# Performance work log

Measured on AMD Instinct MI355X. Metric: run time of the kernel, lower is better.

Reference implementation:

```python
import jax, jax.numpy as jnp
import numpy as np

B, S, D, H = 4, 2048, 1024, 16
DH = D // H  # 64
EPS = 1e-5


def setup_inputs() -> dict:
    key = jax.random.key(0)
    ks = jax.random.split(key, 6)
    scale = 0.02
    return {
        "x": jax.random.normal(ks[0], (B, S, D), dtype=jnp.float32),
        "Wq": jax.random.normal(ks[1], (H, D, DH), dtype=jnp.float32) * scale,
        "Wk": jax.random.normal(ks[2], (H, D, DH), dtype=jnp.float32) * scale,
        "Wv": jax.random.normal(ks[3], (H, D, DH), dtype=jnp.float32) * scale,
        "Wo": jax.random.normal(ks[4], (D, D), dtype=jnp.float32) * scale,
        "bo": jnp.zeros((D,), dtype=jnp.float32),
        "gamma": jnp.ones((D,), dtype=jnp.float32),
        "beta": jnp.zeros((D,), dtype=jnp.float32),
    }


def reference(x, Wq, Wk, Wv, Wo, bo, gamma, beta):
    # Per-head projections, stacked across heads: [B,H,S,DH]
    q = jnp.einsum("bsd,hdk->bhsk", x, Wq)
    k = jnp.einsum("bsd,hdk->bhsk", x, Wk)
    v = jnp.einsum("bsd,hdk->bhsk", x, Wv)
    inv_scale = 1.0 / jnp.sqrt(jnp.float32(DH))  # key.size(-1) == head_dim
    scores = jnp.einsum("bhqk,bhsk->bhqs", q, k) * inv_scale  # [B,H,S,S]
    attn = jax.nn.softmax(scores, axis=-1)
    ctx = jnp.einsum("bhqs,bhsk->bhqk", attn, v)  # [B,H,S,DH]
    # concat heads -> [B,S,D]
    concat = jnp.transpose(ctx, (0, 2, 1, 3)).reshape(B, S, D)
    proj = concat @ Wo + bo  # fc_out (Wo stored as [in,out])
    added = proj + x  # residual add
    mu = jnp.mean(added, axis=-1, keepdims=True)
    var = jnp.mean(jnp.square(added - mu), axis=-1, keepdims=True)
    normed = (added - mu) * jax.lax.rsqrt(var + EPS)
    return normed * gamma + beta
```

## Files before the change

### kernel.cpp

```cpp
#include <hip/hip_runtime.h>
#include <hip/hip_bf16.h>
#include <stdint.h>

#define DEV __device__ __forceinline__

typedef short s16x8 __attribute__((ext_vector_type(8)));
typedef float f32x4 __attribute__((ext_vector_type(4)));
typedef int i32x4 __attribute__((ext_vector_type(4)));

DEV void async_load16(const void* g, void* l) {
  __builtin_amdgcn_global_load_lds((void __attribute__((address_space(1)))*)(g),
                                   (void __attribute__((address_space(3)))*)(l),
                                   16, 0, 0);
}

DEV unsigned pack_bf16x2(float a, float b) {
  __hip_bfloat162 h = __float22bfloat162_rn(make_float2(a, b));
  union { __hip_bfloat162 h2; unsigned u; } cv;
  cv.h2 = h;
  return cv.u;
}

__global__ __launch_bounds__(256) void cast_x_kernel(const float* __restrict__ in,
                                                     __hip_bfloat16* __restrict__ out, int n4) {
  int i = blockIdx.x * 256 + threadIdx.x;
  if (i >= n4) return;
  float4 v = ((const float4*)in)[i];
  alignas(8) __hip_bfloat16 t[4] = {__float2bfloat16(v.x), __float2bfloat16(v.y),
                                    __float2bfloat16(v.z), __float2bfloat16(v.w)};
  *(uint2*)(out + (size_t)i * 4) = *(const uint2*)t;
}

__global__ __launch_bounds__(256) void transpose_cast_kernel(const float* __restrict__ src,
                                                             __hip_bfloat16* __restrict__ dst,
                                                             int R, int C, float scale) {
  __shared__ float tile[64][65];
  const int r0 = blockIdx.x * 64, c0 = blockIdx.y * 64, bt = blockIdx.z;
  const int tc = threadIdx.x & 63, tr = threadIdx.x >> 6;
  const float* sp = src + (size_t)bt * R * C;
#pragma unroll
  for (int rr = 0; rr < 64; rr += 4)
    tile[tr + rr][tc] = sp[(size_t)(r0 + tr + rr) * C + c0 + tc];
  __syncthreads();
  __hip_bfloat16* dp = dst + (size_t)bt * R * C;
#pragma unroll
  for (int rr = 0; rr < 64; rr += 4) {
    int cc = tr + rr;
    dp[(size_t)(c0 + cc) * R + r0 + tc] = __float2bfloat16(tile[tc][cc] * scale);
  }
}

__global__ __launch_bounds__(256) void qkv_transpose_kernel(const float* __restrict__ Wq,
                                                            const float* __restrict__ Wk,
                                                            const float* __restrict__ Wv,
                                                            __hip_bfloat16* __restrict__ dst,
                                                            float qscale) {
  __shared__ float tile[64][65];
  const int z = blockIdx.z, which = z >> 4, bt = z & 15;
  const int r0 = blockIdx.x * 64;
  const int tc = threadIdx.x & 63, tr = threadIdx.x >> 6;
  const float* src = (which == 0) ? Wq : (which == 1) ? Wk : Wv;
  const float scale = (which == 0) ? qscale : 1.0f;
  const float* sp = src + (size_t)bt * 1024 * 64;
#pragma unroll
  for (int rr = 0; rr < 64; rr += 4)
    tile[tr + rr][tc] = sp[(size_t)(r0 + tr + rr) * 64 + tc];
  __syncthreads();
  __hip_bfloat16* dp = dst + (size_t)z * 1024 * 64;
#pragma unroll
  for (int rr = 0; rr < 64; rr += 4) {
    int cc = tr + rr;
    dp[(size_t)(cc)*1024 + r0 + tc] = __float2bfloat16(tile[tc][cc] * scale);
  }
}

template <int MODE>
__global__ __launch_bounds__(256) void gemm128(const __hip_bfloat16* __restrict__ A,
                                               const __hip_bfloat16* __restrict__ Bt,
                                               void* __restrict__ out0,
                                               void* __restrict__ out1,
                                               void* __restrict__ out2,
                                               const float* __restrict__ bias,
                                               const float* __restrict__ resid,
                                               int M, int N, int K) {
  __shared__ __hip_bfloat16 As[128 * 32];
  __shared__ __hip_bfloat16 Bs[128 * 32];
  const int tid = threadIdx.x;
  const int lane = tid & 63, w = tid >> 6;
  const int lr = lane & 15, lq = lane >> 4;
  const int wm = w >> 1, wn = w & 1;
  const int nlin = blockIdx.x + gridDim.x * blockIdx.y;
  const int xcd = nlin & 7, slot = nlin >> 3;
  const int bx = slot >> 3;
  const int by = xcd * 8 + (slot & 7);
  const int m0 = by * 128, n0 = bx * 128;

  const f32x4 fz = {0.f, 0.f, 0.f, 0.f};
  f32x4 acc[4][4];
#pragma unroll
  for (int i = 0; i < 4; i++)
#pragma unroll
    for (int j = 0; j < 4; j++) acc[i][j] = fz;

  const int kiters = K >> 5;
  for (int kt = 0; kt < kiters; kt++) {
    __syncthreads();
#pragma unroll
    for (int r = 0; r < 2; r++) {
      const int c = r * 256 + tid;
      const int row = c >> 2, kc = c & 3;
      async_load16((const short*)A + (size_t)(m0 + row) * K + kt * 32 + kc * 8,
                   (char*)As + (r * 256 + (tid & 0xC0)) * 16);
      async_load16((const short*)Bt + (size_t)(n0 + row) * K + kt * 32 + kc * 8,
                   (char*)Bs + (r * 256 + (tid & 0xC0)) * 16);
    }
    __syncthreads();
    const short* Ap = (const short*)As;
    const short* Bp = (const short*)Bs;
    s16x8 av[4], bv[4];
#pragma unroll
    for (int i = 0; i < 4; i++)
      av[i] = *(const s16x8*)(Ap + (wm * 64 + i * 16 + lr) * 32 + lq * 8);
#pragma unroll
    for (int j = 0; j < 4; j++)
      bv[j] = *(const s16x8*)(Bp + (wn * 64 + j * 16 + lr) * 32 + lq * 8);
#pragma unroll
    for (int i = 0; i < 4; i++)
#pragma unroll
      for (int j = 0; j < 4; j++)
        acc[i][j] = __builtin_amdgcn_mfma_f32_16x16x32_bf16(av[i], bv[j], acc[i][j], 0, 0, 0);
  }

  if constexpr (MODE == 0) {
    if (n0 < 2048) {
      __hip_bfloat16* dst01 = (__hip_bfloat16*)((n0 < 1024) ? out0 : out1);
#pragma unroll
      for (int i = 0; i < 4; i++)
#pragma unroll
        for (int j = 0; j < 4; j++)
#pragma unroll
          for (int r = 0; r < 4; r++) {
            const int row = m0 + wm * 64 + i * 16 + lq * 4 + r;
            const int col = n0 + wn * 64 + j * 16 + lr;
            const int bb = row >> 11, s = row & 2047;
            const int colq = col & 1023;
            dst01[((((size_t)bb * 16 + (colq >> 6)) * 2048 + s) << 6) + (col & 63)] =
                __float2bfloat16(acc[i][j][r]);
          }
    } else {
#pragma unroll
      for (int i = 0; i < 4; i++)
#pragma unroll
        for (int j = 0; j < 4; j++) {
          const int row0 = m0 + wm * 64 + i * 16 + lq * 4;
          const int col = (n0 - 2048) + wn * 64 + j * 16 + lr;
          const int bb = row0 >> 11, s0 = row0 & 2047;
          alignas(8) __hip_bfloat16 t4[4] = {
              __float2bfloat16(acc[i][j][0]), __float2bfloat16(acc[i][j][1]),
              __float2bfloat16(acc[i][j][2]), __float2bfloat16(acc[i][j][3])};
          *(uint2*)((__hip_bfloat16*)out2 + (size_t)bb * 2097152 + (size_t)col * 2048 + s0) =
              *(const uint2*)t4;
        }
    }
  } else {
#pragma unroll
    for (int i = 0; i < 4; i++)
#pragma unroll
      for (int j = 0; j < 4; j++)
#pragma unroll
        for (int r = 0; r < 4; r++) {
          const int row = m0 + wm * 64 + i * 16 + lq * 4 + r;
          const int col = n0 + wn * 64 + j * 16 + lr;
          const size_t idx = (size_t)row * 1024 + col;
          ((float*)out0)[idx] = acc[i][j][r] + bias[col] + resid[idx];
        }
  }
}

__global__ __launch_bounds__(256, 4) void flash_kernel(const __hip_bfloat16* __restrict__ Qg,
                                                       const __hip_bfloat16* __restrict__ Kg,
                                                       const __hip_bfloat16* __restrict__ Vtg,
                                                       __hip_bfloat16* __restrict__ Og) {
  __shared__ alignas(16) char smem[32768];
  float* xch = (float*)smem;
  const int tid = threadIdx.x;
  const int lane = tid & 63, w = tid >> 6;
  const int lr = lane & 15, lq = lane >> 4;
  const int qp = w >> 1;
  const int kvh = w & 1;
  const int hb = blockIdx.x, qt = blockIdx.y;
  const int h = hb >> 2, b = hb & 3;
  const size_t bh = (size_t)b * 16 + h;
  const short* Qbase = (const short*)Qg + (bh * 2048 + (size_t)qt * 64) * 64;
  const short* Kbh = (const short*)Kg + bh * 2048 * 64;
  const short* Vbh = (const short*)Vtg + bh * 64 * 2048;

  const int rbase = (lr >> 2) * 8 + (lr & 3);
  const int gk = lr & 7;

  s16x8 qb[2][2];
#pragma unroll
  for (int ntl = 0; ntl < 2; ntl++)
#pragma unroll
    for (int ks = 0; ks < 2; ks++)
      qb[ntl][ks] =
          *(const s16x8*)(Qbase + ((qp * 2 + ntl) * 16 + lr) * 64 + ks * 32 + lq * 8);

  s16x8 vones;
#pragma unroll
  for (int e = 0; e < 8; e++) vones[e] = (short)0x3F80;

  const f32x4 fz = {0.f, 0.f, 0.f, 0.f};
  f32x4 o[2][4];
  f32x4 ol[2];
#pragma unroll
  for (int i = 0; i < 2; i++) {
    ol[i] = fz;
#pragma unroll
    for (int j = 0; j < 4; j++) o[i][j] = fz;
  }

  auto stage = [&](int sel, int kb) {
    char* Kl = smem + sel * 16384;
    char* Vl = Kl + 8192;
    const short* Ksrc = Kbh + kb * 64 * 64;
#pragma unroll
    for (int r = 0; r < 2; r++) {
      int c = r * 256 + tid;
      int row = c >> 3, ck = c & 7;
      int g = (row & 3) | (((row >> 3) & 1) << 2);
      async_load16(Ksrc + row * 64 + (ck ^ g) * 8, Kl + (r * 256 + (tid & 0xC0)) * 16);
    }
#pragma unroll
    for (int r = 0; r < 2; r++) {
      int c = r * 256 + tid;
      int row = c >> 3, ck = c & 7;
      async_load16(Vbh + (size_t)row * 2048 + kb * 64 + ((ck ^ (row & 7))) * 8,
                   Vl + (r * 256 + (tid & 0xC0)) * 16);
    }
  };

  stage(0, 0);
  __syncthreads();

  for (int kb = 0; kb < 32; kb++) {
    const int cur = kb & 1;
    if (kb + 1 < 32) stage(cur ^ 1, kb + 1);

    const short* Kp = (const short*)(smem + cur * 16384);
    const short* Vp = (const short*)(smem + cur * 16384 + 8192);

    union { i32x4 i; s16x8 s; } pa[2];
#pragma unroll
    for (int mt = 0; mt < 2; mt++) {
      const int kvrow = kvh * 32 + mt * 4 + rbase;
      s16x8 kf0 = *(const s16x8*)(Kp + kvrow * 64 + (((0 * 4 + lq) ^ gk)) * 8);
      s16x8 kf1 = *(const s16x8*)(Kp + kvrow * 64 + (((1 * 4 + lq) ^ gk)) * 8);
#pragma unroll
      for (int ntl = 0; ntl < 2; ntl++) {
        f32x4 st = fz;
        st = __builtin_amdgcn_mfma_f32_16x16x32_bf16(kf0, qb[ntl][0], st, 0, 0, 0);
        st = __builtin_amdgcn_mfma_f32_16x16x32_bf16(kf1, qb[ntl][1], st, 0, 0, 0);
        float e0 = __builtin_amdgcn_exp2f(st[0]);
        float e1 = __builtin_amdgcn_exp2f(st[1]);
        float e2 = __builtin_amdgcn_exp2f(st[2]);
        float e3 = __builtin_amdgcn_exp2f(st[3]);
        pa[ntl].i[mt * 2 + 0] = (int)pack_bf16x2(e0, e1);
        pa[ntl].i[mt * 2 + 1] = (int)pack_bf16x2(e2, e3);
      }
    }
    __builtin_amdgcn_s_setprio(1);
#pragma unroll
    for (int ntl = 0; ntl < 2; ntl++)
      ol[ntl] = __builtin_amdgcn_mfma_f32_16x16x32_bf16(pa[ntl].s, vones, ol[ntl], 0, 0, 0);
#pragma unroll
    for (int ndh = 0; ndh < 4; ndh++) {
      int vrow = ndh * 16 + lr;
      s16x8 vb = *(const s16x8*)(Vp + vrow * 64 + (((kvh * 4 + lq) ^ (vrow & 7))) * 8);
#pragma unroll
      for (int ntl = 0; ntl < 2; ntl++)
        o[ntl][ndh] =
            __builtin_amdgcn_mfma_f32_16x16x32_bf16(pa[ntl].s, vb, o[ntl][ndh], 0, 0, 0);
    }
    __builtin_amdgcn_s_setprio(0);

    __syncthreads();
  }

  float* slot = xch + w * 1280;
  if (kvh == 0) {
#pragma unroll
    for (int ndh = 0; ndh < 4; ndh++)
      *(f32x4*)(slot + ndh * 256 + lane * 4) = o[1][ndh];
    *(f32x4*)(slot + 1024 + lane * 4) = ol[1];
  } else {
#pragma unroll
    for (int ndh = 0; ndh < 4; ndh++)
      *(f32x4*)(slot + ndh * 256 + lane * 4) = o[0][ndh];
    *(f32x4*)(slot + 1024 + lane * 4) = ol[0];
  }
  __syncthreads();
  const float* ps = xch + (w ^ 1) * 1280;
  if (kvh == 0) {
#pragma unroll
    for (int ndh = 0; ndh < 4; ndh++)
      o[0][ndh] += *(const f32x4*)(ps + ndh * 256 + lane * 4);
    f32x4 lt = ol[0] + *(const f32x4*)(ps + 1024 + lane * 4);
#pragma unroll
    for (int r = 0; r < 4; r++) {
      float inv = __builtin_amdgcn_rcpf(lt[r]);
      int rowg = qt * 64 + w * 16 + lq * 4 + r;
#pragma unroll
      for (int ndh = 0; ndh < 4; ndh++)
        Og[((size_t)b * 2048 + rowg) * 1024 + h * 64 + ndh * 16 + lr] =
            __float2bfloat16(o[0][ndh][r] * inv);
    }
  } else {
#pragma unroll
    for (int ndh = 0; ndh < 4; ndh++)
      o[1][ndh] += *(const f32x4*)(ps + ndh * 256 + lane * 4);
    f32x4 lt = ol[1] + *(const f32x4*)(ps + 1024 + lane * 4);
#pragma unroll
    for (int r = 0; r < 4; r++) {
      float inv = __builtin_amdgcn_rcpf(lt[r]);
      int rowg = qt * 64 + w * 16 + lq * 4 + r;
#pragma unroll
      for (int ndh = 0; ndh < 4; ndh++)
        Og[((size_t)b * 2048 + rowg) * 1024 + h * 64 + ndh * 16 + lr] =
            __float2bfloat16(o[1][ndh][r] * inv);
    }
  }
}

__global__ __launch_bounds__(256) void ln_kernel(const float* __restrict__ tmp,
                                                 const float* __restrict__ gamma,
                                                 const float* __restrict__ beta,
                                                 float* __restrict__ out) {
  const int row = blockIdx.x, tid = threadIdx.x;
  const int lane = tid & 63, w = tid >> 6;
  const float* rp = tmp + (size_t)row * 1024;
  float4 v = ((const float4*)rp)[tid];
  float s = v.x + v.y + v.z + v.w;
  float ss = v.x * v.x + v.y * v.y + v.z * v.z + v.w * v.w;
#pragma unroll
  for (int off = 32; off >= 1; off >>= 1) {
    s += __shfl_xor(s, off);
    ss += __shfl_xor(ss, off);
  }
  __shared__ float red[8];
  if (lane == 0) {
    red[w] = s;
    red[4 + w] = ss;
  }
  __syncthreads();
  s = red[0] + red[1] + red[2] + red[3];
  ss = red[4] + red[5] + red[6] + red[7];
  const float mu = s * (1.0f / 1024.0f);
  const float var = ss * (1.0f / 1024.0f) - mu * mu;
  const float rstd = rsqrtf(var + 1e-5f);
  float4 g = ((const float4*)gamma)[tid];
  float4 be = ((const float4*)beta)[tid];
  float4 ov;
  ov.x = (v.x - mu) * rstd * g.x + be.x;
  ov.y = (v.y - mu) * rstd * g.y + be.y;
  ov.z = (v.z - mu) * rstd * g.z + be.z;
  ov.w = (v.w - mu) * rstd * g.w + be.w;
  ((float4*)(out + (size_t)row * 1024))[tid] = ov;
}

extern "C" void kernel_launch(void* const* d_in, const int* in_sizes, int n_in,
                              void* d_out, int out_size, void* d_ws, size_t ws_size,
                              hipStream_t stream) {
  (void)in_sizes; (void)n_in; (void)out_size; (void)ws_size;
  const float* x = (const float*)d_in[0];
  const float* Wq = (const float*)d_in[1];
  const float* Wk = (const float*)d_in[2];
  const float* Wv = (const float*)d_in[3];
  const float* Wo = (const float*)d_in[4];
  const float* bo = (const float*)d_in[5];
  const float* gamma = (const float*)d_in[6];
  const float* beta = (const float*)d_in[7];
  float* out = (float*)d_out;
  char* ws = (char*)d_ws;

  __hip_bfloat16* xb = (__hip_bfloat16*)(ws + 0);
  __hip_bfloat16* wqkvT = (__hip_bfloat16*)(ws + 16777216);
  __hip_bfloat16* woT = (__hip_bfloat16*)(ws + 23068672);
  __hip_bfloat16* Q = (__hip_bfloat16*)(ws + 25165824);
  __hip_bfloat16* Kt = (__hip_bfloat16*)(ws + 41943040);
  __hip_bfloat16* Vt = (__hip_bfloat16*)(ws + 58720256);
  __hip_bfloat16* cc = (__hip_bfloat16*)(ws + 75497472);
  float* tmp = (float*)(ws + 25165824);

  cast_x_kernel<<<8192, 256, 0, stream>>>(x, xb, 2097152);
  qkv_transpose_kernel<<<dim3(16, 1, 48), 256, 0, stream>>>(Wq, Wk, Wv, wqkvT,
                                                            0.125f * 1.44269504088896f);
  transpose_cast_kernel<<<dim3(16, 16, 1), 256, 0, stream>>>(Wo, woT, 1024, 1024, 1.0f);

  gemm128<0><<<dim3(24, 64), 256, 0, stream>>>(xb, wqkvT, Q, Kt, Vt, nullptr, nullptr,
                                               8192, 3072, 1024);

  flash_kernel<<<dim3(64, 32), 256, 0, stream>>>(Q, Kt, Vt, cc);

  gemm128<2><<<dim3(8, 64), 256, 0, stream>>>(cc, woT, tmp, nullptr, nullptr, bo, x,
                                              8192, 1024, 1024);
  ln_kernel<<<8192, 256, 0, stream>>>(tmp, gamma, beta, out);
}
```

Before: 303.2 us.

## Double-buffer GEMM LDS tiles with staggered per-wave compute phases

Converts the 128x128 bf16 GEMM main loop from single-buffered load-then-compute into a double-buffered pipeline. Each k-iteration is split into four barrier-separated phases. Each phase issues one sub-tile of the next iteration's loads, and only the wave whose operands have landed (tracked with vmcnt(2)) runs its MFMAs, at raised priority. The aim is to overlap global-to-LDS async loads with MFMA work and avoid full-tile waits. The cost is twice the LDS per block, four barriers per iteration, and MFMA work serialized across waves within a block.

```diff
diff --git a/kernel.cpp b/kernel.cpp
--- a/kernel.cpp
+++ b/kernel.cpp
@@ -83,8 +83,8 @@
                                                const float* __restrict__ bias,
                                                const float* __restrict__ resid,
                                                int M, int N, int K) {
-  __shared__ __hip_bfloat16 As[128 * 32];
-  __shared__ __hip_bfloat16 Bs[128 * 32];
+  __shared__ __hip_bfloat16 As[2][128 * 32];
+  __shared__ __hip_bfloat16 Bs[2][128 * 32];
   const int tid = threadIdx.x;
   const int lane = tid & 63, w = tid >> 6;
   const int lr = lane & 15, lq = lane >> 4;
@@ -102,21 +102,21 @@
 #pragma unroll
     for (int j = 0; j < 4; j++) acc[i][j] = fz;
 
-  const int kiters = K >> 5;
-  for (int kt = 0; kt < kiters; kt++) {
-    __syncthreads();
-#pragma unroll
-    for (int r = 0; r < 2; r++) {
-      const int c = r * 256 + tid;
-      const int row = c >> 2, kc = c & 3;
-      async_load16((const short*)A + (size_t)(m0 + row) * K + kt * 32 + kc * 8,
-                   (char*)As + (r * 256 + (tid & 0xC0)) * 16);
-      async_load16((const short*)Bt + (size_t)(n0 + row) * K + kt * 32 + kc * 8,
-                   (char*)Bs + (r * 256 + (tid & 0xC0)) * 16);
-    }
-    __syncthreads();
-    const short* Ap = (const short*)As;
-    const short* Bp = (const short*)Bs;
+  auto stageA = [&](int sel, int kt, int r) {
+    const int c = r * 256 + tid;
+    const int row = c >> 2, kc = c & 3;
+    async_load16((const short*)A + (size_t)(m0 + row) * K + kt * 32 + kc * 8,
+                 (char*)As[sel] + (r * 256 + (tid & 0xC0)) * 16);
+  };
+  auto stageB = [&](int sel, int kt, int r) {
+    const int c = r * 256 + tid;
+    const int row = c >> 2, kc = c & 3;
+    async_load16((const short*)Bt + (size_t)(n0 + row) * K + kt * 32 + kc * 8,
+                 (char*)Bs[sel] + (r * 256 + (tid & 0xC0)) * 16);
+  };
+  auto compute = [&](int cur) {
+    const short* Ap = (const short*)As[cur];
+    const short* Bp = (const short*)Bs[cur];
     s16x8 av[4], bv[4];
 #pragma unroll
     for (int i = 0; i < 4; i++)
@@ -124,11 +124,44 @@
 #pragma unroll
     for (int j = 0; j < 4; j++)
       bv[j] = *(const s16x8*)(Bp + (wn * 64 + j * 16 + lr) * 32 + lq * 8);
+    __builtin_amdgcn_s_setprio(1);
 #pragma unroll
     for (int i = 0; i < 4; i++)
 #pragma unroll
       for (int j = 0; j < 4; j++)
         acc[i][j] = __builtin_amdgcn_mfma_f32_16x16x32_bf16(av[i], bv[j], acc[i][j], 0, 0, 0);
+    __builtin_amdgcn_s_setprio(0);
+  };
+
+  const int kiters = K >> 5;
+  stageA(0, 0, 0);
+  stageB(0, 0, 0);
+  stageB(0, 0, 1);
+  stageA(0, 0, 1);
+
+  for (int kt = 0; kt < kiters; kt++) {
+    const int cur = kt & 1, nxt = cur ^ 1;
+    const int ktn = (kt + 1 < kiters) ? kt + 1 : kt;
+    asm volatile("s_waitcnt vmcnt(2)" ::: "memory");
+    __builtin_amdgcn_s_barrier();
+    __builtin_amdgcn_sched_barrier(0);
+    stageA(nxt, ktn, 0);
+    if (w == 0) compute(cur);
+    asm volatile("s_waitcnt vmcnt(2)" ::: "memory");
+    __builtin_amdgcn_s_barrier();
+    __builtin_amdgcn_sched_barrier(0);
+    stageB(nxt, ktn, 0);
+    if (w == 1) compute(cur);
+    asm volatile("s_waitcnt vmcnt(2)" ::: "memory");
+    __builtin_amdgcn_s_barrier();
+    __builtin_amdgcn_sched_barrier(0);
+    stageB(nxt, ktn, 1);
+    if (w == 2) compute(cur);
+    asm volatile("s_waitcnt vmcnt(2)" ::: "memory");
+    __builtin_amdgcn_s_barrier();
+    __builtin_amdgcn_sched_barrier(0);
+    stageA(nxt, ktn, 1);
+    if (w == 3) compute(cur);
   }
 
   if constexpr (MODE == 0) {
```

Result: slower. 359.0 us (+18.4%).

## Double GEMM K-tile and single-buffer flash kernel for higher occupancy

Applied to the files above, without the earlier changes.

The GEMM kernel now stages a 64-wide K slice per iteration instead of 32, halving the number of barrier-separated load/compute rounds and issuing twice as many MFMAs between syncs. The flash attention kernel drops its double-buffered K/V staging in favour of a single buffer, shrinks LDS, and raises the launch-bounds occupancy hint from 4 to 7 blocks. This trades explicit prefetch overlap in attention for more resident waves to hide latency, and it risks losing load/compute overlap plus register pressure under the tighter bound.

```diff
diff --git a/kernel.cpp b/kernel.cpp
--- a/kernel.cpp
+++ b/kernel.cpp
@@ -83,8 +83,8 @@
                                                const float* __restrict__ bias,
                                                const float* __restrict__ resid,
                                                int M, int N, int K) {
-  __shared__ __hip_bfloat16 As[128 * 32];
-  __shared__ __hip_bfloat16 Bs[128 * 32];
+  __shared__ __hip_bfloat16 As[128 * 64];
+  __shared__ __hip_bfloat16 Bs[128 * 64];
   const int tid = threadIdx.x;
   const int lane = tid & 63, w = tid >> 6;
   const int lr = lane & 15, lq = lane >> 4;
@@ -102,33 +102,40 @@
 #pragma unroll
     for (int j = 0; j < 4; j++) acc[i][j] = fz;
 
-  const int kiters = K >> 5;
+  const int kiters = K >> 6;
   for (int kt = 0; kt < kiters; kt++) {
     __syncthreads();
 #pragma unroll
-    for (int r = 0; r < 2; r++) {
+    for (int r = 0; r < 4; r++) {
       const int c = r * 256 + tid;
-      const int row = c >> 2, kc = c & 3;
-      async_load16((const short*)A + (size_t)(m0 + row) * K + kt * 32 + kc * 8,
+      const int row = c >> 3, ck = c & 7;
+      async_load16((const short*)A + (size_t)(m0 + row) * K + kt * 64 + ck * 8,
                    (char*)As + (r * 256 + (tid & 0xC0)) * 16);
-      async_load16((const short*)Bt + (size_t)(n0 + row) * K + kt * 32 + kc * 8,
+      async_load16((const short*)Bt + (size_t)(n0 + row) * K + kt * 64 + ck * 8,
                    (char*)Bs + (r * 256 + (tid & 0xC0)) * 16);
     }
     __syncthreads();
     const short* Ap = (const short*)As;
     const short* Bp = (const short*)Bs;
-    s16x8 av[4], bv[4];
+    s16x8 av[4][2], bv[4][2];
 #pragma unroll
     for (int i = 0; i < 4; i++)
-      av[i] = *(const s16x8*)(Ap + (wm * 64 + i * 16 + lr) * 32 + lq * 8);
+#pragma unroll
+      for (int ks = 0; ks < 2; ks++)
+        av[i][ks] = *(const s16x8*)(Ap + (wm * 64 + i * 16 + lr) * 64 + ks * 32 + lq * 8);
 #pragma unroll
     for (int j = 0; j < 4; j++)
-      bv[j] = *(const s16x8*)(Bp + (wn * 64 + j * 16 + lr) * 32 + lq * 8);
-#pragma unroll
-    for (int i = 0; i < 4; i++)
-#pragma unroll
-      for (int j = 0; j < 4; j++)
-        acc[i][j] = __builtin_amdgcn_mfma_f32_16x16x32_bf16(av[i], bv[j], acc[i][j], 0, 0, 0);
+#pragma unroll
+      for (int ks = 0; ks < 2; ks++)
+        bv[j][ks] = *(const s16x8*)(Bp + (wn * 64 + j * 16 + lr) * 64 + ks * 32 + lq * 8);
+#pragma unroll
+    for (int ks = 0; ks < 2; ks++)
+#pragma unroll
+      for (int i = 0; i < 4; i++)
+#pragma unroll
+        for (int j = 0; j < 4; j++)
+          acc[i][j] =
+              __builtin_amdgcn_mfma_f32_16x16x32_bf16(av[i][ks], bv[j][ks], acc[i][j], 0, 0, 0);
   }
 
   if constexpr (MODE == 0) {
@@ -177,11 +184,11 @@
   }
 }
 
-__global__ __launch_bounds__(256, 4) void flash_kernel(const __hip_bfloat16* __restrict__ Qg,
+__global__ __launch_bounds__(256, 7) void flash_kernel(const __hip_bfloat16* __restrict__ Qg,
                                                        const __hip_bfloat16* __restrict__ Kg,
                                                        const __hip_bfloat16* __restrict__ Vtg,
                                                        __hip_bfloat16* __restrict__ Og) {
-  __shared__ alignas(16) char smem[32768];
+  __shared__ alignas(16) char smem[20480];
   float* xch = (float*)smem;
   const int tid = threadIdx.x;
   const int lane = tid & 63, w = tid >> 6;
@@ -220,9 +227,9 @@
     for (int j = 0; j < 4; j++) o[i][j] = fz;
   }
 
-  auto stage = [&](int sel, int kb) {
-    char* Kl = smem + sel * 16384;
-    char* Vl = Kl + 8192;
+  auto stage = [&](int kb) {
+    char* Kl = smem;
+    char* Vl = smem + 8192;
     const short* Ksrc = Kbh + kb * 64 * 64;
 #pragma unroll
     for (int r = 0; r < 2; r++) {
@@ -240,15 +247,12 @@
     }
   };
 
-  stage(0, 0);
-  __syncthreads();
-
   for (int kb = 0; kb < 32; kb++) {
-    const int cur = kb & 1;
-    if (kb + 1 < 32) stage(cur ^ 1, kb + 1);
-
-    const short* Kp = (const short*)(smem + cur * 16384);
-    const short* Vp = (const short*)(smem + cur * 16384 + 8192);
+    stage(kb);
+    __syncthreads();
+
+    const short* Kp = (const short*)smem;
+    const short* Vp = (const short*)(smem + 8192);
 
     union { i32x4 i; s16x8 s; } pa[2];
 #pragma unroll
```

Result: slower. 669.2 us (+120.7%).

## Replace QKV projection GEMM with 256x128 triple-buffered async-LDS pipelined kernel

Applied to the files above, without the earlier changes.

Adds a dedicated QKV GEMM with 256x128 tiles, 512 threads, a 64-wide K step and three LDS stages. Global-to-LDS loads are XOR-swizzled to avoid bank conflicts and are split so A and B loads interleave with MFMA halves. Blocks are remapped so each XCD works on its own band of rows, and MFMA sections run at raised wave priority. The aim is to hide memory latency and improve reuse in the largest GEMM, at the cost of more LDS per block (144 KB) and lower occupancy.

```diff
diff --git a/kernel.cpp b/kernel.cpp
--- a/kernel.cpp
+++ b/kernel.cpp
@@ -71,6 +71,140 @@
   for (int rr = 0; rr < 64; rr += 4) {
     int cc = tr + rr;
     dp[(size_t)(cc)*1024 + r0 + tc] = __float2bfloat16(tile[tc][cc] * scale);
+  }
+}
+
+__global__ __launch_bounds__(512, 2) void gemm256_qkv(const __hip_bfloat16* __restrict__ A,
+                                                      const __hip_bfloat16* __restrict__ Bt,
+                                                      __hip_bfloat16* __restrict__ outQ,
+                                                      __hip_bfloat16* __restrict__ outK,
+                                                      __hip_bfloat16* __restrict__ outV,
+                                                      int M, int N, int K) {
+  __shared__ __hip_bfloat16 lds[3 * 24576];
+  const int tid = threadIdx.x;
+  const int lane = tid & 63, w = tid >> 6;
+  const int lr = lane & 15, lq = lane >> 4;
+  const int wm = w >> 1, wn = w & 1;
+  const int gk = lr & 7;
+  const int nlin = blockIdx.x + gridDim.x * blockIdx.y;
+  const int xcd = nlin & 7, sid = nlin >> 3;
+  const int bx = sid >> 2;
+  const int by = xcd * 4 + (sid & 3);
+  const int m0 = by * 256, n0 = bx * 128;
+
+  const f32x4 fz = {0.f, 0.f, 0.f, 0.f};
+  f32x4 acc[4][4];
+#pragma unroll
+  for (int i = 0; i < 4; i++)
+#pragma unroll
+    for (int j = 0; j < 4; j++) acc[i][j] = fz;
+
+  auto stageA = [&](int tt, int sl) {
+#pragma unroll
+    for (int r = 0; r < 4; r++) {
+      const int c = r * 512 + tid;
+      const int row = c >> 3, ck = c & 7;
+      async_load16((const short*)A + (size_t)(m0 + row) * K + tt * 64 + ((ck ^ (row & 7)) * 8),
+                   (char*)lds + sl * 49152 + (r * 512 + (tid & 0x1C0)) * 16);
+    }
+  };
+  auto stageB = [&](int tt, int sl) {
+#pragma unroll
+    for (int r = 0; r < 2; r++) {
+      const int c = r * 512 + tid;
+      const int row = c >> 3, ck = c & 7;
+      async_load16((const short*)Bt + (size_t)(n0 + row) * K + tt * 64 + ((ck ^ (row & 7)) * 8),
+                   (char*)lds + sl * 49152 + 32768 + (r * 512 + (tid & 0x1C0)) * 16);
+    }
+  };
+
+  stageA(0, 0); stageB(0, 0);
+  stageA(1, 1); stageB(1, 1);
+
+  const int kiters = K >> 6;
+  int slot = 0;
+  for (int t = 0; t < kiters; t++) {
+    const short* Ap = (const short*)lds + slot * 24576;
+    const short* Bp = Ap + 16384;
+    const int tt = (t + 2 < kiters) ? t + 2 : kiters - 1;
+    int sln = slot + 2; if (sln >= 3) sln -= 3;
+
+    asm volatile("s_waitcnt vmcnt(6)\n\ts_barrier" ::: "memory");
+
+    stageA(tt, sln);
+    s16x8 bv[4][2], av0[2][2];
+#pragma unroll
+    for (int j = 0; j < 4; j++)
+#pragma unroll
+      for (int ks = 0; ks < 2; ks++)
+        bv[j][ks] = *(const s16x8*)(Bp + (wn * 64 + j * 16 + lr) * 64 + (((ks * 4 + lq) ^ gk)) * 8);
+#pragma unroll
+    for (int i = 0; i < 2; i++)
+#pragma unroll
+      for (int ks = 0; ks < 2; ks++)
+        av0[i][ks] = *(const s16x8*)(Ap + (wm * 64 + i * 16 + lr) * 64 + (((ks * 4 + lq) ^ gk)) * 8);
+    __builtin_amdgcn_s_setprio(1);
+#pragma unroll
+    for (int ks = 0; ks < 2; ks++)
+#pragma unroll
+      for (int i = 0; i < 2; i++)
+#pragma unroll
+      for (int j = 0; j < 4; j++)
+        acc[i][j] = __builtin_amdgcn_mfma_f32_16x16x32_bf16(av0[i][ks], bv[j][ks], acc[i][j], 0, 0, 0);
+    __builtin_amdgcn_s_setprio(0);
+    asm volatile("s_barrier" ::: "memory");
+
+    stageB(tt, sln);
+    s16x8 av1[2][2];
+#pragma unroll
+    for (int i = 0; i < 2; i++)
+#pragma unroll
+      for (int ks = 0; ks < 2; ks++)
+        av1[i][ks] =
+            *(const s16x8*)(Ap + (wm * 64 + (2 + i) * 16 + lr) * 64 + (((ks * 4 + lq) ^ gk)) * 8);
+    __builtin_amdgcn_s_setprio(1);
+#pragma unroll
+    for (int ks = 0; ks < 2; ks++)
+#pragma unroll
+      for (int i = 0; i < 2; i++)
+#pragma unroll
+      for (int j = 0; j < 4; j++)
+        acc[2 + i][j] =
+            __builtin_amdgcn_mfma_f32_16x16x32_bf16(av1[i][ks], bv[j][ks], acc[2 + i][j], 0, 0, 0);
+    __builtin_amdgcn_s_setprio(0);
+    asm volatile("s_barrier" ::: "memory");
+
+    slot = slot + 1; if (slot == 3) slot = 0;
+  }
+
+  if (n0 < 2048) {
+    __hip_bfloat16* dst01 = (n0 < 1024) ? outQ : outK;
+#pragma unroll
+    for (int i = 0; i < 4; i++)
+#pragma unroll
+      for (int j = 0; j < 4; j++)
+#pragma unroll
+        for (int r = 0; r < 4; r++) {
+          const int row = m0 + wm * 64 + i * 16 + lq * 4 + r;
+          const int col = n0 + wn * 64 + j * 16 + lr;
+          const int bb = row >> 11, s = row & 2047;
+          const int colq = col & 1023;
+          dst01[((((size_t)bb * 16 + (colq >> 6)) * 2048 + s) << 6) + (col & 63)] =
+              __float2bfloat16(acc[i][j][r]);
+        }
+  } else {
+#pragma unroll
+    for (int i = 0; i < 4; i++)
+#pragma unroll
+      for (int j = 0; j < 4; j++) {
+        const int row0 = m0 + wm * 64 + i * 16 + lq * 4;
+        const int col = (n0 - 2048) + wn * 64 + j * 16 + lr;
+        const int bb = row0 >> 11, s0 = row0 & 2047;
+        alignas(8) __hip_bfloat16 t4[4] = {
+            __float2bfloat16(acc[i][j][0]), __float2bfloat16(acc[i][j][1]),
+            __float2bfloat16(acc[i][j][2]), __float2bfloat16(acc[i][j][3])};
+        *(uint2*)(outV + (size_t)bb * 2097152 + (size_t)col * 2048 + s0) = *(const uint2*)t4;
+      }
   }
 }
 
@@ -131,50 +265,17 @@
         acc[i][j] = __builtin_amdgcn_mfma_f32_16x16x32_bf16(av[i], bv[j], acc[i][j], 0, 0, 0);
   }
 
-  if constexpr (MODE == 0) {
-    if (n0 < 2048) {
-      __hip_bfloat16* dst01 = (__hip_bfloat16*)((n0 < 1024) ? out0 : out1);
-#pragma unroll
-      for (int i = 0; i < 4; i++)
-#pragma unroll
-        for (int j = 0; j < 4; j++)
-#pragma unroll
-          for (int r = 0; r < 4; r++) {
-            const int row = m0 + wm * 64 + i * 16 + lq * 4 + r;
-            const int col = n0 + wn * 64 + j * 16 + lr;
-            const int bb = row >> 11, s = row & 2047;
-            const int colq = col & 1023;
-            dst01[((((size_t)bb * 16 + (colq >> 6)) * 2048 + s) << 6) + (col & 63)] =
-                __float2bfloat16(acc[i][j][r]);
-          }
-    } else {
-#pragma unroll
-      for (int i = 0; i < 4; i++)
-#pragma unroll
-        for (int j = 0; j < 4; j++) {
-          const int row0 = m0 + wm * 64 + i * 16 + lq * 4;
-          const int col = (n0 - 2048) + wn * 64 + j * 16 + lr;
-          const int bb = row0 >> 11, s0 = row0 & 2047;
-          alignas(8) __hip_bfloat16 t4[4] = {
-              __float2bfloat16(acc[i][j][0]), __float2bfloat16(acc[i][j][1]),
-              __float2bfloat16(acc[i][j][2]), __float2bfloat16(acc[i][j][3])};
-          *(uint2*)((__hip_bfloat16*)out2 + (size_t)bb * 2097152 + (size_t)col * 2048 + s0) =
-              *(const uint2*)t4;
-        }
-    }
-  } else {
-#pragma unroll
-    for (int i = 0; i < 4; i++)
-#pragma unroll
-      for (int j = 0; j < 4; j++)
-#pragma unroll
-        for (int r = 0; r < 4; r++) {
-          const int row = m0 + wm * 64 + i * 16 + lq * 4 + r;
-          const int col = n0 + wn * 64 + j * 16 + lr;
-          const size_t idx = (size_t)row * 1024 + col;
-          ((float*)out0)[idx] = acc[i][j][r] + bias[col] + resid[idx];
-        }
-  }
+#pragma unroll
+  for (int i = 0; i < 4; i++)
+#pragma unroll
+    for (int j = 0; j < 4; j++)
+#pragma unroll
+      for (int r = 0; r < 4; r++) {
+        const int row = m0 + wm * 64 + i * 16 + lq * 4 + r;
+        const int col = n0 + wn * 64 + j * 16 + lr;
+        const size_t idx = (size_t)row * 1024 + col;
+        ((float*)out0)[idx] = acc[i][j][r] + bias[col] + resid[idx];
+      }
 }
 
 __global__ __launch_bounds__(256, 4) void flash_kernel(const __hip_bfloat16* __restrict__ Qg,
@@ -397,8 +498,7 @@
                                                             0.125f * 1.44269504088896f);
   transpose_cast_kernel<<<dim3(16, 16, 1), 256, 0, stream>>>(Wo, woT, 1024, 1024, 1.0f);
 
-  gemm128<0><<<dim3(24, 64), 256, 0, stream>>>(xb, wqkvT, Q, Kt, Vt, nullptr, nullptr,
-                                               8192, 3072, 1024);
+  gemm256_qkv<<<dim3(24, 32), 512, 0, stream>>>(xb, wqkvT, Q, Kt, Vt, 8192, 3072, 1024);
 
   flash_kernel<<<dim3(64, 32), 256, 0, stream>>>(Q, Kt, Vt, cc);
 
```

After: 296.2 us. 1.02x faster.
